# Kernel tuning notes

Hardware: AMD Instinct MI355X
Metric: run time of the kernel (lower is better)

Reference implementation:

```python
import jax, jax.numpy as jnp
import numpy as np

N = 50000        # nodes
E = 800000       # edges (before self-loops)
F_IN = 128       # num_features
HID = 32         # hidden_size per head
HEADS = 4
CLS = 40         # num_classes
NEG_SLOPE = 0.2  # PyG GATConv default leaky_relu slope


def setup_inputs() -> dict:
    key = jax.random.key(0)
    ks = jax.random.split(key, 10)
    s = lambda k, sh: (jax.random.normal(k, sh, jnp.float32) * 0.05)
    x = jax.random.normal(ks[0], (N, F_IN), jnp.float32)
    edge_index = jax.random.randint(ks[1], (2, E), 0, N, dtype=jnp.int64)
    W1 = s(ks[2], (F_IN, HEADS * HID))
    att_src1 = s(ks[3], (HEADS, HID))
    att_dst1 = s(ks[4], (HEADS, HID))
    b1 = jnp.zeros((HEADS * HID,), jnp.float32)
    W2 = s(ks[5], (HEADS * HID, CLS))
    att_src2 = s(ks[6], (1, CLS))
    att_dst2 = s(ks[7], (1, CLS))
    b2 = jnp.zeros((CLS,), jnp.float32)
    return {"x": x, "edge_index": edge_index, "W1": W1, "att_src1": att_src1,
            "att_dst1": att_dst1, "b1": b1, "W2": W2, "att_src2": att_src2,
            "att_dst2": att_dst2, "b2": b2}


def _add_self_loops(edge_index, num_nodes):
    ar = jnp.arange(num_nodes, dtype=edge_index.dtype)
    loops = jnp.stack([ar, ar])
    return jnp.concatenate([edge_index, loops], axis=1)


def _gat_conv(x, edge_index, W, a_src, a_dst, bias, heads, concat):
    """PyG GATConv (eval mode, additive attention, self-loops already added)."""
    n = x.shape[0]
    src, dst = edge_index[0], edge_index[1]
    h = (x @ W).reshape(n, heads, -1)                 # [N, H, C]
    a_s = jnp.einsum('nhc,hc->nh', h, a_src)          # [N, H]
    a_d = jnp.einsum('nhc,hc->nh', h, a_dst)          # [N, H]
    e = jax.nn.leaky_relu(a_s[src] + a_d[dst], NEG_SLOPE)   # [E', H]
    m = jax.ops.segment_max(e, dst, num_segments=n)   # segment softmax over dst
    ex = jnp.exp(e - m[dst])
    den = jax.ops.segment_sum(ex, dst, num_segments=n)
    alpha = ex / den[dst]                             # [E', H]
    out = jax.ops.segment_sum(h[src] * alpha[:, :, None], dst, num_segments=n)
    out = out.reshape(n, -1) if concat else out.mean(axis=1)
    return out + bias


def reference(x, edge_index, W1, att_src1, att_dst1, b1, W2, att_src2, att_dst2, b2):
    ei = _add_self_loops(edge_index, x.shape[0])
    # dropout p=0 in eval -> identity
    h = jax.nn.relu(_gat_conv(x, ei, W1, att_src1, att_dst1, b1, HEADS, True))
    out = _gat_conv(h, ei, W2, att_src2, att_dst2, b2, 1, True)  # heads=1
    return out
```

## Files before the change

### kernel.cpp

```cpp
#include <hip/hip_runtime.h>
#include <cstdint>

#define NODES 50000
#define FIN   128
#define C1    128
#define HEADS 4
#define HID   32
#define CLS   40
#define SLOPE 0.2f

#define NBUCK ((NODES + 255) >> 8)
#define EPB 2048
#define BCAP 8192

__device__ __forceinline__ float lrelu(float v) { return v > 0.f ? v : SLOPE * v; }

__device__ __forceinline__ unsigned short f2bf(float f) {
    union { float f; unsigned u; } v; v.f = f;
    unsigned u = v.u;
    return (unsigned short)((u + 0x7FFFu + ((u >> 16) & 1u)) >> 16);
}
__device__ __forceinline__ float bf2f(unsigned short b) {
    union { unsigned u; float f; } v; v.u = ((unsigned)b) << 16;
    return v.f;
}
__device__ __forceinline__ float bflo(unsigned u) {
    union { unsigned x; float f; } v; v.x = u << 16; return v.f;
}
__device__ __forceinline__ float bfhi(unsigned u) {
    union { unsigned x; float f; } v; v.x = u & 0xffff0000u; return v.f;
}
__device__ __forceinline__ unsigned cvtpk(float a, float b) {
    unsigned r;
    asm("v_cvt_pk_bf16_f32 %0, %1, %2" : "=v"(r) : "v"(a), "v"(b));
    return r;
}

typedef __attribute__((ext_vector_type(8))) short bf16x8;
typedef __attribute__((ext_vector_type(4))) float f32x4;
typedef __attribute__((ext_vector_type(4), aligned(4))) int int4a;
typedef __attribute__((ext_vector_type(2), aligned(4))) int int2a;

__device__ __forceinline__ void acc8(float w, uint4 p, float* ac) {
    ac[0] = fmaf(w, bflo(p.x), ac[0]); ac[1] = fmaf(w, bfhi(p.x), ac[1]);
    ac[2] = fmaf(w, bflo(p.y), ac[2]); ac[3] = fmaf(w, bfhi(p.y), ac[3]);
    ac[4] = fmaf(w, bflo(p.z), ac[4]); ac[5] = fmaf(w, bfhi(p.z), ac[5]);
    ac[6] = fmaf(w, bflo(p.w), ac[6]); ac[7] = fmaf(w, bfhi(p.w), ac[7]);
}

__global__ __launch_bounds__(256) void k_prep(const float* __restrict__ W1,
                                              const float* __restrict__ W2,
                                              unsigned short* __restrict__ w1t,
                                              unsigned short* __restrict__ w2t,
                                              int* __restrict__ bwp) {
    const int b = blockIdx.x, t = threadIdx.x;
    if (b < 8) {
        __shared__ unsigned short Tb[16][136];
        const int n0 = b * 16;
        const int k = t & 127, g = t >> 7;
#pragma unroll
        for (int i = 0; i < 8; i++)
            Tb[g * 8 + i][k] = f2bf(W1[(size_t)k * C1 + n0 + g * 8 + i]);
        __syncthreads();
        {
            int nl = t >> 4, k8 = (t & 15) * 8;
            *(uint4*)(w1t + (n0 + nl) * 128 + k8) = *(uint4*)(&Tb[nl][k8]);
        }
    } else {
        for (int p = t; p < CLS * 128; p += 256) {
            int n = p >> 7, k = p & 127;
            w2t[n * 128 + k] = f2bf(W2[(size_t)k * CLS + n]);
        }
        if (t < NBUCK) bwp[t] = t * BCAP;
    }
}

__global__ __launch_bounds__(256) void k_front(const float* __restrict__ X,
                                               const unsigned short* __restrict__ w1t,
                                               const float* __restrict__ AS,
                                               const float* __restrict__ AD,
                                               unsigned short* __restrict__ h1b,
                                               float* __restrict__ as1,
                                               float* __restrict__ ad1,
                                               const int* __restrict__ src,
                                               const int* __restrict__ dst, int E,
                                               int* __restrict__ bwp,
                                               int* __restrict__ tmp, int GB1) {
    __shared__ unsigned short Asm[64][136];
    __shared__ unsigned short Wt[128][136];
    __shared__ int cnt[NBUCK];
    __shared__ int bbs[NBUCK];
    const int t = threadIdx.x;

    if (blockIdx.x >= GB1) {
        for (int i = t; i < NBUCK; i += 256) cnt[i] = 0;
        __syncthreads();
        const int e0 = (blockIdx.x - GB1) * EPB;
        int v[8], rb[8];
#pragma unroll
        for (int k = 0; k < 8; k++) {
            int e = e0 + k * 256 + t;
            rb[k] = -1;
            if (e < E) {
                int d = dst[e], s = src[e];
                int b = d >> 8;
                int r = atomicAdd(&cnt[b], 1);
                v[k] = (s << 8) | (d & 255);
                rb[k] = (r << 8) | b;
            }
        }
        __syncthreads();
        for (int i = t; i < NBUCK; i += 256) {
            int c = cnt[i];
            bbs[i] = c ? atomicAdd(&bwp[i], c) : 0;
        }
        __syncthreads();
#pragma unroll
        for (int k = 0; k < 8; k++) {
            if (rb[k] >= 0) {
                int b = rb[k] & 255;
                int r = rb[k] >> 8;
                tmp[bbs[b] + r] = v[k];
            }
        }
        return;
    }

    const int row0 = blockIdx.x * 64;
#pragma unroll
    for (int i = 0; i < 8; i++) {
        int p = i * 256 + t;
        int n = p >> 4, k8 = (p & 15) * 8;
        *(uint4*)(&Wt[n][k8]) = *(const uint4*)(w1t + n * 128 + k8);
    }
    {
        int r = t >> 2, c0 = (t & 3) * 32;
        int gr = row0 + r;
        if (gr < NODES) {
#pragma unroll
            for (int i = 0; i < 4; i++) {
                float4 va = *(const float4*)(X + (size_t)gr * FIN + c0 + i * 8);
                float4 vb = *(const float4*)(X + (size_t)gr * FIN + c0 + i * 8 + 4);
                uint4 pk;
                pk.x = cvtpk(va.x, va.y);
                pk.y = cvtpk(va.z, va.w);
                pk.z = cvtpk(vb.x, vb.y);
                pk.w = cvtpk(vb.z, vb.w);
                *(uint4*)(&Asm[r][c0 + i * 8]) = pk;
            }
        } else {
            uint4 z = make_uint4(0, 0, 0, 0);
#pragma unroll
            for (int i = 0; i < 4; i++) *(uint4*)(&Asm[r][c0 + i * 8]) = z;
        }
    }
    __syncthreads();

    const int w = t >> 6, l = t & 63;
    const int lm = l & 15, quad = l >> 4;
    f32x4 acc[8];
#pragma unroll
    for (int ct = 0; ct < 8; ct++) acc[ct] = (f32x4){0.f, 0.f, 0.f, 0.f};
#pragma unroll
    for (int kt = 0; kt < 4; kt++) {
        bf16x8 a = *(const bf16x8*)(&Asm[w * 16 + lm][kt * 32 + quad * 8]);
#pragma unroll
        for (int ct = 0; ct < 8; ct++) {
            bf16x8 b = *(const bf16x8*)(&Wt[ct * 16 + lm][kt * 32 + quad * 8]);
            acc[ct] = __builtin_amdgcn_mfma_f32_16x16x32_bf16(a, b, acc[ct], 0, 0, 0);
        }
    }
    __syncthreads();
#pragma unroll
    for (int ct = 0; ct < 8; ct++)
#pragma unroll
        for (int r = 0; r < 4; r++)
            Asm[w * 16 + quad * 4 + r][ct * 16 + lm] = f2bf(acc[ct][r]);
    __syncthreads();
    {
        int r = t >> 2, c0 = (t & 3) * 32;
        int gr = row0 + r;
        if (gr < NODES) {
#pragma unroll
            for (int i = 0; i < 4; i++)
                *(uint4*)(h1b + (size_t)gr * C1 + c0 + i * 8) =
                    *(uint4*)(&Asm[r][c0 + i * 8]);
        }
    }
    {
        int r = t >> 2, h = t & 3;
        int gr = row0 + r;
        if (gr < NODES) {
            float s = 0.f, d = 0.f;
#pragma unroll
            for (int j = 0; j < 32; j++) {
                float v = bf2f(Asm[r][h * 32 + j]);
                s = fmaf(v, AS[h * HID + j], s);
                d = fmaf(v, AD[h * HID + j], d);
            }
            as1[gr * HEADS + h] = s;
            ad1[gr * HEADS + h] = d;
        }
    }
}

__global__ __launch_bounds__(256) void k_bucketB(const int* __restrict__ bwp,
                                                 const int* __restrict__ tmp,
                                                 int* __restrict__ col,
                                                 int* __restrict__ rowptr,
                                                 int* __restrict__ degarr) {
    __shared__ int degs[256];
    __shared__ int wp[256];
    __shared__ int wsum[4];
    const int b = blockIdx.x, t = threadIdx.x;
    const int n0 = b << 8;
    const int beg = b * BCAP;
    const int end = bwp[b];
    degs[t] = 0;
    __syncthreads();
    for (int e = beg + t; e < end; e += 256)
        atomicAdd(&degs[tmp[e] & 255], 1);
    __syncthreads();
    const int d = degs[t];
    int incl = d;
    const int lane = t & 63, w = t >> 6;
#pragma unroll
    for (int s = 1; s < 64; s <<= 1) {
        int u = __shfl_up(incl, s);
        if (lane >= s) incl += u;
    }
    if (lane == 63) wsum[w] = incl;
    __syncthreads();
    if (t == 0) {
        int r = 0;
#pragma unroll
        for (int i = 0; i < 4; i++) { int x = wsum[i]; wsum[i] = r; r += x; }
    }
    __syncthreads();
    const int excl = incl - d + wsum[w] + beg;
    const int nidx = n0 + t;
    if (nidx < NODES) { rowptr[nidx] = excl; degarr[nidx] = d; }
    wp[t] = excl;
    __syncthreads();
    for (int e = beg + t; e < end; e += 256) {
        int v = tmp[e];
        int p = atomicAdd(&wp[v & 255], 1);
        col[p] = v >> 8;
    }
}

__global__ __launch_bounds__(256) void k_agg1(const unsigned short* __restrict__ h1b,
                                              const float* __restrict__ as1,
                                              const float* __restrict__ ad1,
                                              const int* __restrict__ rowptr,
                                              const int* __restrict__ degarr,
                                              const int* __restrict__ col,
                                              const float* __restrict__ b1,
                                              unsigned short* __restrict__ out1) {
    int wid = (blockIdx.x * 256 + threadIdx.x) >> 6;
    if (wid >= NODES) return;
    const int lane = threadIdx.x & 63;
    const int q  = lane >> 4;
    const int ll = lane & 15;
    const int fh = ll >> 2;
    const int n = wid;
    const float adn = ad1[n * HEADS + fh];
    const int rs = rowptr[n];
    const int re = rs + degarr[n];
    const unsigned lo = (unsigned)(ll << 4);

    float den = 0.f;
    float ac[8];
#pragma unroll
    for (int k = 0; k < 8; k++) ac[k] = 0.f;

    int base = rs;
    for (; re - base > 16; base += 32) {
        int4a ca = *(const int4a*)(col + base + q * 4);
        int4a cb = *(const int4a*)(col + base + 16 + q * 4);
        const int ia = base + q * 4;
        const int ib = base + 16 + q * 4;
        int c0 = (ia + 0 < re) ? ca.x : n;
        int c1 = (ia + 1 < re) ? ca.y : n;
        int c2 = (ia + 2 < re) ? ca.z : n;
        int c3 = (ia + 3 < re) ? ca.w : n;
        int c4 = (ib + 0 < re) ? cb.x : n;
        int c5 = (ib + 1 < re) ? cb.y : n;
        int c6 = (ib + 2 < re) ? cb.z : n;
        int c7 = (ib + 3 < re) ? cb.w : n;
        float w0 = __expf(lrelu(as1[c0 * HEADS + fh] + adn)); if (ia + 0 >= re) w0 = 0.f;
        float w1 = __expf(lrelu(as1[c1 * HEADS + fh] + adn)); if (ia + 1 >= re) w1 = 0.f;
        float w2 = __expf(lrelu(as1[c2 * HEADS + fh] + adn)); if (ia + 2 >= re) w2 = 0.f;
        float w3 = __expf(lrelu(as1[c3 * HEADS + fh] + adn)); if (ia + 3 >= re) w3 = 0.f;
        float w4 = __expf(lrelu(as1[c4 * HEADS + fh] + adn)); if (ib + 0 >= re) w4 = 0.f;
        float w5 = __expf(lrelu(as1[c5 * HEADS + fh] + adn)); if (ib + 1 >= re) w5 = 0.f;
        float w6 = __expf(lrelu(as1[c6 * HEADS + fh] + adn)); if (ib + 2 >= re) w6 = 0.f;
        float w7 = __expf(lrelu(as1[c7 * HEADS + fh] + adn)); if (ib + 3 >= re) w7 = 0.f;
        den += ((w0 + w1) + (w2 + w3)) + ((w4 + w5) + (w6 + w7));
        uint4 p0 = *(const uint4*)((const char*)h1b + (((unsigned)c0 << 8) + lo));
        uint4 p1 = *(const uint4*)((const char*)h1b + (((unsigned)c1 << 8) + lo));
        uint4 p2 = *(const uint4*)((const char*)h1b + (((unsigned)c2 << 8) + lo));
        uint4 p3 = *(const uint4*)((const char*)h1b + (((unsigned)c3 << 8) + lo));
        uint4 p4 = *(const uint4*)((const char*)h1b + (((unsigned)c4 << 8) + lo));
        uint4 p5 = *(const uint4*)((const char*)h1b + (((unsigned)c5 << 8) + lo));
        uint4 p6 = *(const uint4*)((const char*)h1b + (((unsigned)c6 << 8) + lo));
        uint4 p7 = *(const uint4*)((const char*)h1b + (((unsigned)c7 << 8) + lo));
        acc8(w0, p0, ac); acc8(w1, p1, ac); acc8(w2, p2, ac); acc8(w3, p3, ac);
        acc8(w4, p4, ac); acc8(w5, p5, ac); acc8(w6, p6, ac); acc8(w7, p7, ac);
    }
    if (base < re) {
        int4a ca = *(const int4a*)(col + base + q * 4);
        const int ia = base + q * 4;
        int c0 = (ia + 0 < re) ? ca.x : n;
        int c1 = (ia + 1 < re) ? ca.y : n;
        int c2 = (ia + 2 < re) ? ca.z : n;
        int c3 = (ia + 3 < re) ? ca.w : n;
        float w0 = __expf(lrelu(as1[c0 * HEADS + fh] + adn)); if (ia + 0 >= re) w0 = 0.f;
        float w1 = __expf(lrelu(as1[c1 * HEADS + fh] + adn)); if (ia + 1 >= re) w1 = 0.f;
        float w2 = __expf(lrelu(as1[c2 * HEADS + fh] + adn)); if (ia + 2 >= re) w2 = 0.f;
        float w3 = __expf(lrelu(as1[c3 * HEADS + fh] + adn)); if (ia + 3 >= re) w3 = 0.f;
        den += (w0 + w1) + (w2 + w3);
        uint4 p0 = *(const uint4*)((const char*)h1b + (((unsigned)c0 << 8) + lo));
        uint4 p1 = *(const uint4*)((const char*)h1b + (((unsigned)c1 << 8) + lo));
        uint4 p2 = *(const uint4*)((const char*)h1b + (((unsigned)c2 << 8) + lo));
        uint4 p3 = *(const uint4*)((const char*)h1b + (((unsigned)c3 << 8) + lo));
        acc8(w0, p0, ac); acc8(w1, p1, ac); acc8(w2, p2, ac); acc8(w3, p3, ac);
    }
    den += __shfl_xor(den, 16);
    den += __shfl_xor(den, 32);
#pragma unroll
    for (int k = 0; k < 8; k++) {
        ac[k] += __shfl_xor(ac[k], 16);
        ac[k] += __shfl_xor(ac[k], 32);
    }
    const float wself = __expf(lrelu(as1[n * HEADS + fh] + adn));
    den += wself;
    if (q == 0) {
        unsigned offs = ((unsigned)n << 8) + lo;
        uint4 sp = *(const uint4*)((const char*)h1b + offs);
        float sv[8] = {bflo(sp.x), bfhi(sp.x), bflo(sp.y), bfhi(sp.y),
                       bflo(sp.z), bfhi(sp.z), bflo(sp.w), bfhi(sp.w)};
        float4 bv0 = *(const float4*)(b1 + ll * 8);
        float4 bv1 = *(const float4*)(b1 + ll * 8 + 4);
        float bb[8] = {bv0.x, bv0.y, bv0.z, bv0.w, bv1.x, bv1.y, bv1.z, bv1.w};
        const float inv = 1.f / den;
        float o[8];
#pragma unroll
        for (int k = 0; k < 8; k++)
            o[k] = fmaxf(fmaf(wself, sv[k], ac[k]) * inv + bb[k], 0.f);
        uint4 pk;
        pk.x = cvtpk(o[0], o[1]);
        pk.y = cvtpk(o[2], o[3]);
        pk.z = cvtpk(o[4], o[5]);
        pk.w = cvtpk(o[6], o[7]);
        *(uint4*)(out1 + (size_t)n * C1 + ll * 8) = pk;
    }
}

__global__ __launch_bounds__(256) void k_gemm2(const unsigned short* __restrict__ out1b,
                                               const unsigned short* __restrict__ w2t,
                                               const float* __restrict__ AS,
                                               const float* __restrict__ AD,
                                               unsigned short* __restrict__ h2b,
                                               float* __restrict__ as2,
                                               float* __restrict__ ad2) {
    __shared__ unsigned short Asm[64][136];
    __shared__ unsigned short Wt2[48][136];
    __shared__ float Cc[64][52];
    const int t = threadIdx.x;
    const int row0 = blockIdx.x * 64;

    for (int p = t; p < 8 * 136; p += 256) Wt2[40 + p / 136][p % 136] = 0;
    for (int p = t; p < 640; p += 256) {
        int n = p >> 4, k8 = (p & 15) * 8;
        *(uint4*)(&Wt2[n][k8]) = *(const uint4*)(w2t + n * 128 + k8);
    }
    {
        int r = t >> 2, c0 = (t & 3) * 32;
        int gr = row0 + r;
        if (gr < NODES) {
#pragma unroll
            for (int i = 0; i < 4; i++)
                *(uint4*)(&Asm[r][c0 + i * 8]) =
                    *(const uint4*)(out1b + (size_t)gr * C1 + c0 + i * 8);
        } else {
            uint4 z = make_uint4(0, 0, 0, 0);
#pragma unroll
            for (int i = 0; i < 4; i++) *(uint4*)(&Asm[r][c0 + i * 8]) = z;
        }
    }
    __syncthreads();

    const int w = t >> 6, l = t & 63;
    const int lm = l & 15, quad = l >> 4;
    f32x4 acc[3];
#pragma unroll
    for (int ct = 0; ct < 3; ct++) acc[ct] = (f32x4){0.f, 0.f, 0.f, 0.f};
#pragma unroll
    for (int kt = 0; kt < 4; kt++) {
        bf16x8 a = *(const bf16x8*)(&Asm[w * 16 + lm][kt * 32 + quad * 8]);
#pragma unroll
        for (int ct = 0; ct < 3; ct++) {
            bf16x8 b = *(const bf16x8*)(&Wt2[ct * 16 + lm][kt * 32 + quad * 8]);
            acc[ct] = __builtin_amdgcn_mfma_f32_16x16x32_bf16(a, b, acc[ct], 0, 0, 0);
        }
    }
    __syncthreads();
#pragma unroll
    for (int ct = 0; ct < 3; ct++)
#pragma unroll
        for (int r = 0; r < 4; r++)
            Cc[w * 16 + quad * 4 + r][ct * 16 + lm] = acc[ct][r];
    __syncthreads();
    {
        int r = t >> 2, c0 = (t & 3) * 10;
        int gr = row0 + r;
        if (gr < NODES) {
#pragma unroll
            for (int i = 0; i < 5; i++) {
                int c = c0 + i * 2;
                unsigned pk = cvtpk(Cc[r][c], Cc[r][c + 1]);
                *(unsigned*)(h2b + (size_t)gr * 64 + c) = pk;
            }
            float s = 0.f, d = 0.f;
#pragma unroll
            for (int j = 0; j < 10; j++) {
                float v = Cc[r][c0 + j];
                s = fmaf(v, AS[c0 + j], s);
                d = fmaf(v, AD[c0 + j], d);
            }
            s += __shfl_xor(s, 1); s += __shfl_xor(s, 2);
            d += __shfl_xor(d, 1); d += __shfl_xor(d, 2);
            if ((t & 3) == 0) { as2[gr] = s; ad2[gr] = d; }
        }
    }
}

__global__ __launch_bounds__(256) void k_agg2(const unsigned short* __restrict__ h2b,
                                              const float* __restrict__ as2,
                                              const float* __restrict__ ad2,
                                              const int* __restrict__ rowptr,
                                              const int* __restrict__ degarr,
                                              const int* __restrict__ col,
                                              const float* __restrict__ b2,
                                              float* __restrict__ out) {
    int wid = (blockIdx.x * 256 + threadIdx.x) >> 6;
    if (wid >= NODES) return;
    const int lane = threadIdx.x & 63;
    const int q8 = lane >> 3, l8 = lane & 7;
    const int n = wid;
    const float adn = ad2[n];
    const int rs = rowptr[n];
    const int re = rs + degarr[n];
    const unsigned lo = (unsigned)(l8 << 4);

    float den = 0.f;
    float ac[8];
#pragma unroll
    for (int k = 0; k < 8; k++) ac[k] = 0.f;

    int base = rs;
    for (; re - base > 16; base += 32) {
        int4a cc = *(const int4a*)(col + base + q8 * 4);
        const int i0 = base + q8 * 4;
        int c0 = (i0 + 0 < re) ? cc.x : n;
        int c1 = (i0 + 1 < re) ? cc.y : n;
        int c2 = (i0 + 2 < re) ? cc.z : n;
        int c3 = (i0 + 3 < re) ? cc.w : n;
        float w0 = __expf(lrelu(as2[c0] + adn)); if (i0 + 0 >= re) w0 = 0.f;
        float w1 = __expf(lrelu(as2[c1] + adn)); if (i0 + 1 >= re) w1 = 0.f;
        float w2 = __expf(lrelu(as2[c2] + adn)); if (i0 + 2 >= re) w2 = 0.f;
        float w3 = __expf(lrelu(as2[c3] + adn)); if (i0 + 3 >= re) w3 = 0.f;
        den += (w0 + w1) + (w2 + w3);
        if (l8 < 5) {
            uint4 p0 = *(const uint4*)((const char*)h2b + (((unsigned)c0 << 7) + lo));
            uint4 p1 = *(const uint4*)((const char*)h2b + (((unsigned)c1 << 7) + lo));
            uint4 p2 = *(const uint4*)((const char*)h2b + (((unsigned)c2 << 7) + lo));
            uint4 p3 = *(const uint4*)((const char*)h2b + (((unsigned)c3 << 7) + lo));
            acc8(w0, p0, ac); acc8(w1, p1, ac);
            acc8(w2, p2, ac); acc8(w3, p3, ac);
        }
    }
    if (base < re) {
        int2a cc = *(const int2a*)(col + base + q8 * 2);
        const int i0 = base + q8 * 2;
        int c0 = (i0 + 0 < re) ? cc.x : n;
        int c1 = (i0 + 1 < re) ? cc.y : n;
        float w0 = __expf(lrelu(as2[c0] + adn)); if (i0 + 0 >= re) w0 = 0.f;
        float w1 = __expf(lrelu(as2[c1] + adn)); if (i0 + 1 >= re) w1 = 0.f;
        den += w0 + w1;
        if (l8 < 5) {
            uint4 p0 = *(const uint4*)((const char*)h2b + (((unsigned)c0 << 7) + lo));
            uint4 p1 = *(const uint4*)((const char*)h2b + (((unsigned)c1 << 7) + lo));
            acc8(w0, p0, ac); acc8(w1, p1, ac);
        }
    }
    den += __shfl_xor(den, 8);
    den += __shfl_xor(den, 16);
    den += __shfl_xor(den, 32);
#pragma unroll
    for (int k = 0; k < 8; k++) {
        ac[k] += __shfl_xor(ac[k], 8);
        ac[k] += __shfl_xor(ac[k], 16);
        ac[k] += __shfl_xor(ac[k], 32);
    }
    const float wself = __expf(lrelu(as2[n] + adn));
    den += wself;
    if (q8 == 0 && l8 < 5) {
        unsigned offs = ((unsigned)n << 7) + lo;
        uint4 sp = *(const uint4*)((const char*)h2b + offs);
        float sv[8] = {bflo(sp.x), bfhi(sp.x), bflo(sp.y), bfhi(sp.y),
                       bflo(sp.z), bfhi(sp.z), bflo(sp.w), bfhi(sp.w)};
        float4 bv0 = *(const float4*)(b2 + l8 * 8);
        float4 bv1 = *(const float4*)(b2 + l8 * 8 + 4);
        float bb[8] = {bv0.x, bv0.y, bv0.z, bv0.w, bv1.x, bv1.y, bv1.z, bv1.w};
        float o[8];
#pragma unroll
        for (int k = 0; k < 8; k++)
            o[k] = (ac[k] + wself * sv[k]) / den + bb[k];
        *(float4*)(out + (size_t)n * CLS + l8 * 8) =
            make_float4(o[0], o[1], o[2], o[3]);
        *(float4*)(out + (size_t)n * CLS + l8 * 8 + 4) =
            make_float4(o[4], o[5], o[6], o[7]);
    }
}

extern "C" void kernel_launch(void* const* d_in, const int* in_sizes, int n_in,
                              void* d_out, int out_size, void* d_ws, size_t ws_size,
                              hipStream_t stream) {
    const float* x     = (const float*)d_in[0];
    const int*   ei    = (const int*)d_in[1];
    const float* W1    = (const float*)d_in[2];
    const float* aS1   = (const float*)d_in[3];
    const float* aD1   = (const float*)d_in[4];
    const float* b1    = (const float*)d_in[5];
    const float* W2    = (const float*)d_in[6];
    const float* aS2   = (const float*)d_in[7];
    const float* aD2   = (const float*)d_in[8];
    const float* b2    = (const float*)d_in[9];
    float* out = (float*)d_out;
    const int E = in_sizes[1] / 2;
    const int* src = ei;
    const int* dst = ei + E;

    char* ws = (char*)d_ws;
    size_t off = 0;
    auto alloc = [&](size_t bytes) -> char* {
        char* p = ws + off;
        off += (bytes + 255) & ~(size_t)255;
        return p;
    };
    unsigned short* h1b  = (unsigned short*)alloc((size_t)NODES * C1 * 2);
    unsigned short* out1 = (unsigned short*)alloc((size_t)NODES * C1 * 2);
    unsigned short* h2b  = (unsigned short*)alloc((size_t)NODES * 64 * 2);
    float* as1    = (float*)alloc((size_t)NODES * HEADS * 4);
    float* ad1    = (float*)alloc((size_t)NODES * HEADS * 4);
    float* as2    = (float*)alloc((size_t)NODES * 4);
    float* ad2    = (float*)alloc((size_t)NODES * 4);
    int* rowptr   = (int*)alloc((size_t)NODES * 4);
    int* degarr   = (int*)alloc((size_t)NODES * 4);
    int* col      = (int*)alloc((size_t)NBUCK * BCAP * 4 + 256);
    int* tmp      = (int*)alloc((size_t)NBUCK * BCAP * 4 + 256);
    unsigned short* w1t = (unsigned short*)alloc((size_t)FIN * C1 * 2);
    unsigned short* w2t = (unsigned short*)alloc((size_t)CLS * 128 * 2);
    int* bwp      = (int*)alloc((size_t)NBUCK * 4);

    const int GB1 = (NODES + 63) / 64;
    const int GBA = (E + EPB - 1) / EPB;

    k_prep<<<9, 256, 0, stream>>>(W1, W2, w1t, w2t, bwp);
    k_front<<<GB1 + GBA, 256, 0, stream>>>(x, w1t, aS1, aD1, h1b, as1, ad1,
                                           src, dst, E, bwp, tmp, GB1);
    k_bucketB<<<NBUCK, 256, 0, stream>>>(bwp, tmp, col, rowptr, degarr);
    k_agg1<<<(NODES * 64) / 256, 256, 0, stream>>>(h1b, as1, ad1, rowptr, degarr,
                                                   col, b1, out1);
    k_gemm2<<<(NODES + 63) / 64, 256, 0, stream>>>(out1, w2t, aS2, aD2, h2b, as2, ad2);
    k_agg2<<<(NODES * 64) / 256, 256, 0, stream>>>(h2b, as2, ad2, rowptr, degarr,
                                                   col, b2, out);
}
```

Before: 193.7 us.

## Precompute per-edge attention weights in CSR order and compact h2 rows

Computes the exponentiated layer-1 attention weights per edge during the CSR bucket scatter, and adds a new kernel that computes the layer-2 weights per edge, so the aggregation kernels read contiguous weights instead of gathering as[] and calling exp. The h2 feature rows are packed to 40 bf16 values instead of padded 64, which shrinks the gather footprint. The bucket kernel moves to 512 threads and the gemm1 attention dot product is vectorised. This adds extra global traffic for the weight arrays and dloc, plus one more kernel launch.

```diff
diff --git a/kernel.cpp b/kernel.cpp
--- a/kernel.cpp
+++ b/kernel.cpp
@@ -40,6 +40,8 @@
 typedef __attribute__((ext_vector_type(4))) float f32x4;
 typedef __attribute__((ext_vector_type(4), aligned(4))) int int4a;
 typedef __attribute__((ext_vector_type(2), aligned(4))) int int2a;
+typedef __attribute__((ext_vector_type(4), aligned(4))) float f32x4a;
+typedef __attribute__((ext_vector_type(2), aligned(4))) float f32x2a;
 
 __device__ __forceinline__ void acc8(float w, uint4 p, float* ac) {
     ac[0] = fmaf(w, bflo(p.x), ac[0]); ac[1] = fmaf(w, bfhi(p.x), ac[1]);
@@ -193,10 +195,22 @@
         if (gr < NODES) {
             float s = 0.f, d = 0.f;
 #pragma unroll
-            for (int j = 0; j < 32; j++) {
-                float v = bf2f(Asm[r][h * 32 + j]);
-                s = fmaf(v, AS[h * HID + j], s);
-                d = fmaf(v, AD[h * HID + j], d);
+            for (int i = 0; i < 4; i++) {
+                uint4 hv = *(const uint4*)(&Asm[r][h * 32 + i * 8]);
+                float4 a0 = *(const float4*)(AS + h * HID + i * 8);
+                float4 a1 = *(const float4*)(AS + h * HID + i * 8 + 4);
+                float4 d0 = *(const float4*)(AD + h * HID + i * 8);
+                float4 d1 = *(const float4*)(AD + h * HID + i * 8 + 4);
+                float v0 = bflo(hv.x), v1 = bfhi(hv.x), v2 = bflo(hv.y), v3 = bfhi(hv.y);
+                float v4 = bflo(hv.z), v5 = bfhi(hv.z), v6 = bflo(hv.w), v7 = bfhi(hv.w);
+                s = fmaf(v0, a0.x, s); s = fmaf(v1, a0.y, s);
+                s = fmaf(v2, a0.z, s); s = fmaf(v3, a0.w, s);
+                s = fmaf(v4, a1.x, s); s = fmaf(v5, a1.y, s);
+                s = fmaf(v6, a1.z, s); s = fmaf(v7, a1.w, s);
+                d = fmaf(v0, d0.x, d); d = fmaf(v1, d0.y, d);
+                d = fmaf(v2, d0.z, d); d = fmaf(v3, d0.w, d);
+                d = fmaf(v4, d1.x, d); d = fmaf(v5, d1.y, d);
+                d = fmaf(v6, d1.z, d); d = fmaf(v7, d1.w, d);
             }
             as1[gr * HEADS + h] = s;
             ad1[gr * HEADS + h] = d;
@@ -204,32 +218,44 @@
     }
 }
 
-__global__ __launch_bounds__(256) void k_bucketB(const int* __restrict__ bwp,
+__global__ __launch_bounds__(512) void k_bucketB(const int* __restrict__ bwp,
                                                  const int* __restrict__ tmp,
+                                                 const float* __restrict__ as1,
+                                                 const float* __restrict__ ad1,
                                                  int* __restrict__ col,
+                                                 int* __restrict__ dloc,
+                                                 float* __restrict__ wgt1,
                                                  int* __restrict__ rowptr,
                                                  int* __restrict__ degarr) {
     __shared__ int degs[256];
     __shared__ int wp[256];
     __shared__ int wsum[4];
+    __shared__ float Lad[1024];
     const int b = blockIdx.x, t = threadIdx.x;
     const int n0 = b << 8;
     const int beg = b * BCAP;
     const int end = bwp[b];
-    degs[t] = 0;
-    __syncthreads();
-    for (int e = beg + t; e < end; e += 256)
+    if (t < 256) degs[t] = 0;
+    for (int i = t; i < 1024; i += 512) {
+        int gi = n0 * 4 + i;
+        Lad[i] = (gi < NODES * 4) ? ad1[gi] : 0.f;
+    }
+    __syncthreads();
+    for (int e = beg + t; e < end; e += 512)
         atomicAdd(&degs[tmp[e] & 255], 1);
     __syncthreads();
-    const int d = degs[t];
-    int incl = d;
+    int d = 0, incl = 0;
     const int lane = t & 63, w = t >> 6;
-#pragma unroll
-    for (int s = 1; s < 64; s <<= 1) {
-        int u = __shfl_up(incl, s);
-        if (lane >= s) incl += u;
-    }
-    if (lane == 63) wsum[w] = incl;
+    if (t < 256) {
+        d = degs[t];
+        incl = d;
+#pragma unroll
+        for (int s = 1; s < 64; s <<= 1) {
+            int u = __shfl_up(incl, s);
+            if (lane >= s) incl += u;
+        }
+        if (lane == 63) wsum[w] = incl;
+    }
     __syncthreads();
     if (t == 0) {
         int r = 0;
@@ -237,15 +263,27 @@
         for (int i = 0; i < 4; i++) { int x = wsum[i]; wsum[i] = r; r += x; }
     }
     __syncthreads();
-    const int excl = incl - d + wsum[w] + beg;
-    const int nidx = n0 + t;
-    if (nidx < NODES) { rowptr[nidx] = excl; degarr[nidx] = d; }
-    wp[t] = excl;
-    __syncthreads();
-    for (int e = beg + t; e < end; e += 256) {
+    if (t < 256) {
+        const int excl = incl - d + wsum[w] + beg;
+        const int nidx = n0 + t;
+        if (nidx < NODES) { rowptr[nidx] = excl; degarr[nidx] = d; }
+        wp[t] = excl;
+    }
+    __syncthreads();
+    for (int e = beg + t; e < end; e += 512) {
         int v = tmp[e];
-        int p = atomicAdd(&wp[v & 255], 1);
-        col[p] = v >> 8;
+        int dl = v & 255;
+        int s = v >> 8;
+        int p = atomicAdd(&wp[dl], 1);
+        col[p] = s;
+        dloc[p] = dl;
+        float4 a = *(const float4*)(as1 + s * 4);
+        f32x4a wv;
+        wv.x = __expf(lrelu(a.x + Lad[dl * 4 + 0]));
+        wv.y = __expf(lrelu(a.y + Lad[dl * 4 + 1]));
+        wv.z = __expf(lrelu(a.z + Lad[dl * 4 + 2]));
+        wv.w = __expf(lrelu(a.w + Lad[dl * 4 + 3]));
+        *(f32x4a*)(wgt1 + (size_t)p * 4) = wv;
     }
 }
 
@@ -255,6 +293,7 @@
                                               const int* __restrict__ rowptr,
                                               const int* __restrict__ degarr,
                                               const int* __restrict__ col,
+                                              const float* __restrict__ wgt1,
                                               const float* __restrict__ b1,
                                               unsigned short* __restrict__ out1) {
     int wid = (blockIdx.x * 256 + threadIdx.x) >> 6;
@@ -264,7 +303,6 @@
     const int ll = lane & 15;
     const int fh = ll >> 2;
     const int n = wid;
-    const float adn = ad1[n * HEADS + fh];
     const int rs = rowptr[n];
     const int re = rs + degarr[n];
     const unsigned lo = (unsigned)(ll << 4);
@@ -288,14 +326,14 @@
         int c5 = (ib + 1 < re) ? cb.y : n;
         int c6 = (ib + 2 < re) ? cb.z : n;
         int c7 = (ib + 3 < re) ? cb.w : n;
-        float w0 = __expf(lrelu(as1[c0 * HEADS + fh] + adn)); if (ia + 0 >= re) w0 = 0.f;
-        float w1 = __expf(lrelu(as1[c1 * HEADS + fh] + adn)); if (ia + 1 >= re) w1 = 0.f;
-        float w2 = __expf(lrelu(as1[c2 * HEADS + fh] + adn)); if (ia + 2 >= re) w2 = 0.f;
-        float w3 = __expf(lrelu(as1[c3 * HEADS + fh] + adn)); if (ia + 3 >= re) w3 = 0.f;
-        float w4 = __expf(lrelu(as1[c4 * HEADS + fh] + adn)); if (ib + 0 >= re) w4 = 0.f;
-        float w5 = __expf(lrelu(as1[c5 * HEADS + fh] + adn)); if (ib + 1 >= re) w5 = 0.f;
-        float w6 = __expf(lrelu(as1[c6 * HEADS + fh] + adn)); if (ib + 2 >= re) w6 = 0.f;
-        float w7 = __expf(lrelu(as1[c7 * HEADS + fh] + adn)); if (ib + 3 >= re) w7 = 0.f;
+        float w0 = wgt1[(ia + 0) * 4 + fh]; if (ia + 0 >= re) w0 = 0.f;
+        float w1 = wgt1[(ia + 1) * 4 + fh]; if (ia + 1 >= re) w1 = 0.f;
+        float w2 = wgt1[(ia + 2) * 4 + fh]; if (ia + 2 >= re) w2 = 0.f;
+        float w3 = wgt1[(ia + 3) * 4 + fh]; if (ia + 3 >= re) w3 = 0.f;
+        float w4 = wgt1[(ib + 0) * 4 + fh]; if (ib + 0 >= re) w4 = 0.f;
+        float w5 = wgt1[(ib + 1) * 4 + fh]; if (ib + 1 >= re) w5 = 0.f;
+        float w6 = wgt1[(ib + 2) * 4 + fh]; if (ib + 2 >= re) w6 = 0.f;
+        float w7 = wgt1[(ib + 3) * 4 + fh]; if (ib + 3 >= re) w7 = 0.f;
         den += ((w0 + w1) + (w2 + w3)) + ((w4 + w5) + (w6 + w7));
         uint4 p0 = *(const uint4*)((const char*)h1b + (((unsigned)c0 << 8) + lo));
         uint4 p1 = *(const uint4*)((const char*)h1b + (((unsigned)c1 << 8) + lo));
@@ -315,10 +353,10 @@
         int c1 = (ia + 1 < re) ? ca.y : n;
         int c2 = (ia + 2 < re) ? ca.z : n;
         int c3 = (ia + 3 < re) ? ca.w : n;
-        float w0 = __expf(lrelu(as1[c0 * HEADS + fh] + adn)); if (ia + 0 >= re) w0 = 0.f;
-        float w1 = __expf(lrelu(as1[c1 * HEADS + fh] + adn)); if (ia + 1 >= re) w1 = 0.f;
-        float w2 = __expf(lrelu(as1[c2 * HEADS + fh] + adn)); if (ia + 2 >= re) w2 = 0.f;
-        float w3 = __expf(lrelu(as1[c3 * HEADS + fh] + adn)); if (ia + 3 >= re) w3 = 0.f;
+        float w0 = wgt1[(ia + 0) * 4 + fh]; if (ia + 0 >= re) w0 = 0.f;
+        float w1 = wgt1[(ia + 1) * 4 + fh]; if (ia + 1 >= re) w1 = 0.f;
+        float w2 = wgt1[(ia + 2) * 4 + fh]; if (ia + 2 >= re) w2 = 0.f;
+        float w3 = wgt1[(ia + 3) * 4 + fh]; if (ia + 3 >= re) w3 = 0.f;
         den += (w0 + w1) + (w2 + w3);
         uint4 p0 = *(const uint4*)((const char*)h1b + (((unsigned)c0 << 8) + lo));
         uint4 p1 = *(const uint4*)((const char*)h1b + (((unsigned)c1 << 8) + lo));
@@ -333,7 +371,7 @@
         ac[k] += __shfl_xor(ac[k], 16);
         ac[k] += __shfl_xor(ac[k], 32);
     }
-    const float wself = __expf(lrelu(as1[n * HEADS + fh] + adn));
+    const float wself = __expf(lrelu(as1[n * HEADS + fh] + ad1[n * HEADS + fh]));
     den += wself;
     if (q == 0) {
         unsigned offs = ((unsigned)n << 8) + lo;
@@ -420,7 +458,7 @@
             for (int i = 0; i < 5; i++) {
                 int c = c0 + i * 2;
                 unsigned pk = cvtpk(Cc[r][c], Cc[r][c + 1]);
-                *(unsigned*)(h2b + (size_t)gr * 64 + c) = pk;
+                *(unsigned*)(h2b + (size_t)gr * 40 + c) = pk;
             }
             float s = 0.f, d = 0.f;
 #pragma unroll
@@ -436,12 +474,32 @@
     }
 }
 
+__global__ __launch_bounds__(512) void k_wgt2(const int* __restrict__ bwp,
+                                              const int* __restrict__ col,
+                                              const int* __restrict__ dloc,
+                                              const float* __restrict__ as2,
+                                              const float* __restrict__ ad2,
+                                              float* __restrict__ wgt2) {
+    __shared__ float Lad[256];
+    const int b = blockIdx.x, t = threadIdx.x;
+    const int n0 = b << 8;
+    if (t < 256) {
+        int gi = n0 + t;
+        Lad[t] = (gi < NODES) ? ad2[gi] : 0.f;
+    }
+    __syncthreads();
+    const int beg = b * BCAP, end = bwp[b];
+    for (int e = beg + t; e < end; e += 512)
+        wgt2[e] = __expf(lrelu(as2[col[e]] + Lad[dloc[e]]));
+}
+
 __global__ __launch_bounds__(256) void k_agg2(const unsigned short* __restrict__ h2b,
                                               const float* __restrict__ as2,
                                               const float* __restrict__ ad2,
                                               const int* __restrict__ rowptr,
                                               const int* __restrict__ degarr,
                                               const int* __restrict__ col,
+                                              const float* __restrict__ wgt2,
                                               const float* __restrict__ b2,
                                               float* __restrict__ out) {
     int wid = (blockIdx.x * 256 + threadIdx.x) >> 6;
@@ -449,7 +507,6 @@
     const int lane = threadIdx.x & 63;
     const int q8 = lane >> 3, l8 = lane & 7;
     const int n = wid;
-    const float adn = ad2[n];
     const int rs = rowptr[n];
     const int re = rs + degarr[n];
     const unsigned lo = (unsigned)(l8 << 4);
@@ -462,36 +519,38 @@
     int base = rs;
     for (; re - base > 16; base += 32) {
         int4a cc = *(const int4a*)(col + base + q8 * 4);
+        f32x4a wv = *(const f32x4a*)(wgt2 + base + q8 * 4);
         const int i0 = base + q8 * 4;
         int c0 = (i0 + 0 < re) ? cc.x : n;
         int c1 = (i0 + 1 < re) ? cc.y : n;
         int c2 = (i0 + 2 < re) ? cc.z : n;
         int c3 = (i0 + 3 < re) ? cc.w : n;
-        float w0 = __expf(lrelu(as2[c0] + adn)); if (i0 + 0 >= re) w0 = 0.f;
-        float w1 = __expf(lrelu(as2[c1] + adn)); if (i0 + 1 >= re) w1 = 0.f;
-        float w2 = __expf(lrelu(as2[c2] + adn)); if (i0 + 2 >= re) w2 = 0.f;
-        float w3 = __expf(lrelu(as2[c3] + adn)); if (i0 + 3 >= re) w3 = 0.f;
+        float w0 = wv.x; if (i0 + 0 >= re) w0 = 0.f;
+        float w1 = wv.y; if (i0 + 1 >= re) w1 = 0.f;
+        float w2 = wv.z; if (i0 + 2 >= re) w2 = 0.f;
+        float w3 = wv.w; if (i0 + 3 >= re) w3 = 0.f;
         den += (w0 + w1) + (w2 + w3);
         if (l8 < 5) {
-            uint4 p0 = *(const uint4*)((const char*)h2b + (((unsigned)c0 << 7) + lo));
-            uint4 p1 = *(const uint4*)((const char*)h2b + (((unsigned)c1 << 7) + lo));
-            uint4 p2 = *(const uint4*)((const char*)h2b + (((unsigned)c2 << 7) + lo));
-            uint4 p3 = *(const uint4*)((const char*)h2b + (((unsigned)c3 << 7) + lo));
+            uint4 p0 = *(const uint4*)((const char*)h2b + ((unsigned)c0 * 80u + lo));
+            uint4 p1 = *(const uint4*)((const char*)h2b + ((unsigned)c1 * 80u + lo));
+            uint4 p2 = *(const uint4*)((const char*)h2b + ((unsigned)c2 * 80u + lo));
+            uint4 p3 = *(const uint4*)((const char*)h2b + ((unsigned)c3 * 80u + lo));
             acc8(w0, p0, ac); acc8(w1, p1, ac);
             acc8(w2, p2, ac); acc8(w3, p3, ac);
         }
     }
     if (base < re) {
         int2a cc = *(const int2a*)(col + base + q8 * 2);
+        f32x2a wv = *(const f32x2a*)(wgt2 + base + q8 * 2);
         const int i0 = base + q8 * 2;
         int c0 = (i0 + 0 < re) ? cc.x : n;
         int c1 = (i0 + 1 < re) ? cc.y : n;
-        float w0 = __expf(lrelu(as2[c0] + adn)); if (i0 + 0 >= re) w0 = 0.f;
-        float w1 = __expf(lrelu(as2[c1] + adn)); if (i0 + 1 >= re) w1 = 0.f;
+        float w0 = wv.x; if (i0 + 0 >= re) w0 = 0.f;
+        float w1 = wv.y; if (i0 + 1 >= re) w1 = 0.f;
         den += w0 + w1;
         if (l8 < 5) {
-            uint4 p0 = *(const uint4*)((const char*)h2b + (((unsigned)c0 << 7) + lo));
-            uint4 p1 = *(const uint4*)((const char*)h2b + (((unsigned)c1 << 7) + lo));
+            uint4 p0 = *(const uint4*)((const char*)h2b + ((unsigned)c0 * 80u + lo));
+            uint4 p1 = *(const uint4*)((const char*)h2b + ((unsigned)c1 * 80u + lo));
             acc8(w0, p0, ac); acc8(w1, p1, ac);
         }
     }
@@ -504,10 +563,10 @@
         ac[k] += __shfl_xor(ac[k], 16);
         ac[k] += __shfl_xor(ac[k], 32);
     }
-    const float wself = __expf(lrelu(as2[n] + adn));
+    const float wself = __expf(lrelu(as2[n] + ad2[n]));
     den += wself;
     if (q8 == 0 && l8 < 5) {
-        unsigned offs = ((unsigned)n << 7) + lo;
+        unsigned offs = (unsigned)n * 80u + lo;
         uint4 sp = *(const uint4*)((const char*)h2b + offs);
         float sv[8] = {bflo(sp.x), bfhi(sp.x), bflo(sp.y), bfhi(sp.y),
                        bflo(sp.z), bfhi(sp.z), bflo(sp.w), bfhi(sp.w)};
@@ -552,15 +611,18 @@
     };
     unsigned short* h1b  = (unsigned short*)alloc((size_t)NODES * C1 * 2);
     unsigned short* out1 = (unsigned short*)alloc((size_t)NODES * C1 * 2);
-    unsigned short* h2b  = (unsigned short*)alloc((size_t)NODES * 64 * 2);
+    unsigned short* h2b  = (unsigned short*)alloc((size_t)NODES * 40 * 2);
     float* as1    = (float*)alloc((size_t)NODES * HEADS * 4);
     float* ad1    = (float*)alloc((size_t)NODES * HEADS * 4);
     float* as2    = (float*)alloc((size_t)NODES * 4);
     float* ad2    = (float*)alloc((size_t)NODES * 4);
     int* rowptr   = (int*)alloc((size_t)NODES * 4);
     int* degarr   = (int*)alloc((size_t)NODES * 4);
-    int* col      = (int*)alloc((size_t)NBUCK * BCAP * 4 + 256);
-    int* tmp      = (int*)alloc((size_t)NBUCK * BCAP * 4 + 256);
+    int* col      = (int*)alloc((size_t)NBUCK * BCAP * 4 + 1024);
+    int* tmp      = (int*)alloc((size_t)NBUCK * BCAP * 4 + 1024);
+    int* dloc     = (int*)alloc((size_t)NBUCK * BCAP * 4 + 1024);
+    float* wgt1   = (float*)alloc((size_t)NBUCK * BCAP * 16 + 4096);
+    float* wgt2   = (float*)alloc((size_t)NBUCK * BCAP * 4 + 1024);
     unsigned short* w1t = (unsigned short*)alloc((size_t)FIN * C1 * 2);
     unsigned short* w2t = (unsigned short*)alloc((size_t)CLS * 128 * 2);
     int* bwp      = (int*)alloc((size_t)NBUCK * 4);
@@ -571,10 +633,12 @@
     k_prep<<<9, 256, 0, stream>>>(W1, W2, w1t, w2t, bwp);
     k_front<<<GB1 + GBA, 256, 0, stream>>>(x, w1t, aS1, aD1, h1b, as1, ad1,
                                            src, dst, E, bwp, tmp, GB1);
-    k_bucketB<<<NBUCK, 256, 0, stream>>>(bwp, tmp, col, rowptr, degarr);
+    k_bucketB<<<NBUCK, 512, 0, stream>>>(bwp, tmp, as1, ad1, col, dloc, wgt1,
+                                         rowptr, degarr);
     k_agg1<<<(NODES * 64) / 256, 256, 0, stream>>>(h1b, as1, ad1, rowptr, degarr,
-                                                   col, b1, out1);
+                                                   col, wgt1, b1, out1);
     k_gemm2<<<(NODES + 63) / 64, 256, 0, stream>>>(out1, w2t, aS2, aD2, h2b, as2, ad2);
+    k_wgt2<<<NBUCK, 512, 0, stream>>>(bwp, col, dloc, as2, ad2, wgt2);
     k_agg2<<<(NODES * 64) / 256, 256, 0, stream>>>(h2b, as2, ad2, rowptr, degarr,
-                                                   col, b2, out);
-}
+                                                   col, wgt2, b2, out);
+}
```

New measurement: 206.7 us. 1.07x slower.
